# Kernel tuning notes

Hardware: AMD Instinct MI355X
Metric: run time of the kernel (lower is better)

The kernel has to match this reference:

```python
import jax, jax.numpy as jnp
import numpy as np

N_PTS0 = 32   # samples per line
N_PTS1 = 8    # after maxpool (scale factor 4)
DIM_LOI = 128
DIM_FC = 1024
FEAT_DIM = 8
HW = 128      # feature-map spatial size (hardcoded via clamp(max=127) in source)


def setup_inputs() -> dict:
    key = jax.random.key(0)
    ks = jax.random.split(key, 11)
    B, L = 8, 5000
    feature = jax.random.normal(ks[0], (B, 256, HW, HW), jnp.float32)
    # line endpoints in pixel coords [0, 128)
    p = jax.random.uniform(ks[1], (B, L, 2, 2), jnp.float32) * HW
    feat = jax.random.normal(ks[2], (B, L, FEAT_DIM), jnp.float32)
    W_fc1 = jax.random.normal(ks[3], (DIM_LOI, 256), jnp.float32) * 0.05
    b_fc1 = jnp.zeros((DIM_LOI,), jnp.float32)
    d_in = DIM_LOI * N_PTS1 + FEAT_DIM  # 1032
    W1 = jax.random.normal(ks[4], (d_in, DIM_FC), jnp.float32) * 0.03
    b1 = jnp.zeros((DIM_FC,), jnp.float32)
    W2 = jax.random.normal(ks[5], (DIM_FC, DIM_FC), jnp.float32) * 0.03
    b2 = jnp.zeros((DIM_FC,), jnp.float32)
    W3 = jax.random.normal(ks[6], (DIM_FC, 1), jnp.float32) * 0.03
    b3 = jnp.zeros((1,), jnp.float32)
    return dict(feature=feature, p=p, feat=feat, W_fc1=W_fc1, b_fc1=b_fc1,
                W1=W1, b1=b1, W2=W2, b2=b2, W3=W3, b3=b3)


def _loi_head(feature, p, feat, W_fc1, b_fc1, W1, b1, W2, b2, W3, b3):
    B, _, H, W = feature.shape
    L = p.shape[1]
    # fc1: 1x1 conv -> [B, DIM_LOI, H, W]
    x = jnp.einsum('bchw,dc->bdhw', feature, W_fc1) + b_fc1[None, :, None, None]

    # sample N_PTS0 points along each line: [B, L, 32, 2]
    lam = jnp.linspace(0.0, 1.0, N_PTS0, dtype=p.dtype)[:, None]
    pts = p[:, :, 0:1, :] * lam + p[:, :, 1:2, :] * (1.0 - lam) - 0.5
    px, py = pts[..., 0], pts[..., 1]
    px0 = jnp.clip(jnp.floor(px), 0.0, HW - 1)
    py0 = jnp.clip(jnp.floor(py), 0.0, HW - 1)
    px1 = jnp.clip(px0 + 1.0, 0.0, HW - 1)
    py1 = jnp.clip(py0 + 1.0, 0.0, HW - 1)
    px0i, py0i = px0.astype(jnp.int32), py0.astype(jnp.int32)
    px1i, py1i = px1.astype(jnp.int32), py1.astype(jnp.int32)

    # bilinear blend weights [B, L, 32] -> broadcast over channel dim
    w00 = ((px1 - px) * (py1 - py))[:, None]
    w10 = ((px - px0) * (py1 - py))[:, None]
    w01 = ((px1 - px) * (py - py0))[:, None]
    w11 = ((px - px0) * (py - py0))[:, None]

    gather = jax.vmap(lambda xb, ix, iy: xb[:, ix, iy])  # [C,L,32] per image
    xp = (gather(x, px0i, py0i) * w00 + gather(x, px1i, py0i) * w10 +
          gather(x, px0i, py1i) * w01 + gather(x, px1i, py1i) * w11)  # [B,C,L,32]
    xp = jnp.transpose(xp, (0, 2, 1, 3))  # [B, L, C, 32]

    # MaxPool1d(kernel=4, stride=4) over sampled points -> [B, L, C, 8]
    pooled = xp.reshape(B, L, DIM_LOI, N_PTS1, N_PTS0 // N_PTS1).max(-1)
    flat = pooled.reshape(B, L, DIM_LOI * N_PTS1)
    z = jnp.concatenate([flat, feat], axis=-1)  # [B, L, 1032]

    h = jax.nn.relu(z @ W1 + b1)
    h = jax.nn.relu(h @ W2 + b2)
    logits = (h @ W3 + b3)[..., 0]  # [B, L]
    return logits


def reference(feature, p, feat, W_fc1, b_fc1, W1, b1, W2, b2, W3, b3):
    return _loi_head(feature, p, feat, W_fc1, b_fc1, W1, b1, W2, b2, W3, b3)
```

## Files before the change

### kernel.cpp

```cpp
#include <hip/hip_runtime.h>

typedef _Float16 f16;
typedef __fp16 h16x2 __attribute__((ext_vector_type(2)));
typedef f16 f16x8 __attribute__((ext_vector_type(8)));
typedef float f32x4 __attribute__((ext_vector_type(4)));

#define HW    128
#define NPIX  16384
#define CDIM  256
#define DLOI  128
#define LROWS 40000
#define DFC   1024
#define KP1   1088

__global__ __launch_bounds__(256, 4) void conv1x1_kernel(
    const float* __restrict__ feature, const float* __restrict__ Wfc,
    const float* __restrict__ bfc, f16* __restrict__ x) {
  const int tid = threadIdx.x;
  const int l = tid & 63;
  const int w = tid >> 6;
  const int b = blockIdx.y;
  const int pix0 = blockIdx.x * 128;
  const int wr = (w >> 1) * 64;
  const int wc = (w & 1) * 64;
  const int lrow = l & 15;
  const int g4 = l >> 4;

  const float* fb = feature + (size_t)b * CDIM * NPIX;
  f32x4 acc[4][4] = {};

  for (int kf = 0; kf < 8; ++kf) {
    const int kb = kf * 32 + g4 * 8;
    f16x8 bf[4];
#pragma unroll
    for (int n = 0; n < 4; ++n) {
      const float* wp = &Wfc[(size_t)(wc + n * 16 + lrow) * CDIM + kb];
      float4 w0 = *(const float4*)wp;
      float4 w1 = *(const float4*)(wp + 4);
      union { f16x8 v; h16x2 h[4]; } u;
      u.h[0] = __builtin_amdgcn_cvt_pkrtz(w0.x, w0.y);
      u.h[1] = __builtin_amdgcn_cvt_pkrtz(w0.z, w0.w);
      u.h[2] = __builtin_amdgcn_cvt_pkrtz(w1.x, w1.y);
      u.h[3] = __builtin_amdgcn_cvt_pkrtz(w1.z, w1.w);
      bf[n] = u.v;
    }
#pragma unroll
    for (int m = 0; m < 4; ++m) {
      const int pix = pix0 + wr + m * 16 + lrow;
      const float* ap = fb + (size_t)kb * NPIX + pix;
      float av[8];
#pragma unroll
      for (int j = 0; j < 8; ++j) av[j] = ap[(size_t)j * NPIX];
      union { f16x8 v; h16x2 h[4]; } u;
      u.h[0] = __builtin_amdgcn_cvt_pkrtz(av[0], av[1]);
      u.h[1] = __builtin_amdgcn_cvt_pkrtz(av[2], av[3]);
      u.h[2] = __builtin_amdgcn_cvt_pkrtz(av[4], av[5]);
      u.h[3] = __builtin_amdgcn_cvt_pkrtz(av[6], av[7]);
#pragma unroll
      for (int n = 0; n < 4; ++n)
        acc[m][n] = __builtin_amdgcn_mfma_f32_16x16x32_f16(u.v, bf[n], acc[m][n], 0, 0, 0);
    }
  }

#pragma unroll
  for (int m = 0; m < 4; ++m) {
#pragma unroll
    for (int r = 0; r < 4; ++r) {
      const int pix = pix0 + wr + m * 16 + g4 * 4 + r;
      f16* xr = x + ((size_t)b * NPIX + pix) * DLOI;
#pragma unroll
      for (int n = 0; n < 4; ++n) {
        const int d = wc + n * 16 + lrow;
        xr[d] = (f16)(acc[m][n][r] + bfc[d]);
      }
    }
  }
}

__global__ __launch_bounds__(256) void sample_kernel(
    const f16* __restrict__ x, const float* __restrict__ p,
    const float* __restrict__ feat, f16* __restrict__ z) {
  const int tid = threadIdx.x;
  const int wv = tid >> 6;
  const int lane = tid & 63;
  const int sub = lane >> 4;
  const int cl = lane & 15;
  const int bid = blockIdx.x;
  const int b = bid & 7;
  const int row = b * 5000 + (bid >> 3) * 4 + wv;

  const float4 pe = *(const float4*)&p[(size_t)row * 4];
  const size_t bb = (size_t)b * NPIX;
  f16* zr = z + (size_t)row * KP1;

#pragma unroll
  for (int gh = 0; gh < 2; ++gh) {
    const int g = gh * 4 + sub;
    float acc[8];
#pragma unroll
    for (int ci = 0; ci < 8; ++ci) acc[ci] = -1e30f;
#pragma unroll
    for (int pt = 0; pt < 4; ++pt) {
      const int t = g * 4 + pt;
      const float lam = (float)t * (1.0f / 31.0f);
      const float px = pe.x * lam + pe.z * (1.f - lam) - 0.5f;
      const float py = pe.y * lam + pe.w * (1.f - lam) - 0.5f;
      const float px0 = fminf(fmaxf(floorf(px), 0.f), 127.f);
      const float py0 = fminf(fmaxf(floorf(py), 0.f), 127.f);
      const float px1 = fminf(px0 + 1.f, 127.f);
      const float py1 = fminf(py0 + 1.f, 127.f);
      const int ix0 = (int)px0, iy0 = (int)py0, ix1 = (int)px1, iy1 = (int)py1;
      const float w00 = (px1 - px) * (py1 - py);
      const float w10 = (px - px0) * (py1 - py);
      const float w01 = (px1 - px) * (py - py0);
      const float w11 = (px - px0) * (py - py0);

      const f16* r00 = x + (bb + ix0 * HW + iy0) * DLOI + cl * 8;
      const f16* r10 = x + (bb + ix1 * HW + iy0) * DLOI + cl * 8;
      const f16* r01 = x + (bb + ix0 * HW + iy1) * DLOI + cl * 8;
      const f16* r11 = x + (bb + ix1 * HW + iy1) * DLOI + cl * 8;
      f16x8 a  = *(const f16x8*)r00;
      f16x8 bq = *(const f16x8*)r10;
      f16x8 cq = *(const f16x8*)r01;
      f16x8 dq = *(const f16x8*)r11;
#pragma unroll
      for (int ci = 0; ci < 8; ++ci) {
        float m = w00 * (float)a[ci] + w10 * (float)bq[ci] +
                  w01 * (float)cq[ci] + w11 * (float)dq[ci];
        acc[ci] = fmaxf(acc[ci], m);
      }
    }
    f16x8 o;
#pragma unroll
    for (int ci = 0; ci < 8; ++ci) o[ci] = (f16)acc[ci];
    *(f16x8*)(zr + g * 128 + cl * 8) = o;
  }
  if (lane < 8) zr[1024 + lane] = (f16)feat[(size_t)row * 8 + lane];
  else if (lane < 36) *(unsigned int*)((char*)zr + 2064 + (lane - 8) * 4) = 0u;
}

__global__ __launch_bounds__(256) void wtrans_kernel(
    const float* __restrict__ W, f16* __restrict__ Wt, int K, int ldt, int permute) {
  __shared__ float t[32][33];
  const int tx = threadIdx.x & 31, ty = threadIdx.x >> 5;
#pragma unroll
  for (int i = 0; i < 4; ++i) {
    int kd = blockIdx.y * 32 + ty + i * 8;
    int ks = (permute && kd < 1024) ? ((kd & 127) * 8 + (kd >> 7)) : kd;
    int n = blockIdx.x * 32 + tx;
    t[ty + i * 8][tx] = (ks < K) ? W[(size_t)ks * DFC + n] : 0.f;
  }
  __syncthreads();
#pragma unroll
  for (int i = 0; i < 4; ++i) {
    int n = blockIdx.x * 32 + ty + i * 8;
    int k = blockIdx.y * 32 + tx;
    Wt[(size_t)n * ldt + k] = (f16)t[tx][ty + i * 8];
  }
}

__global__ __launch_bounds__(256) void gemm_f16(
    const f16* __restrict__ A, const f16* __restrict__ Bt,
    const float* __restrict__ bias, f16* __restrict__ C,
    int M, int ksteps, int lda) {
  __shared__ f16 As[128 * 64];
  __shared__ f16 Bs[128 * 64];
  const int tid = threadIdx.x;
  const int l = tid & 63;
  const int w = tid >> 6;

  const int nwg = gridDim.x;
  const int s = (blockIdx.x & 7) * (nwg >> 3) + (blockIdx.x >> 3);
  const int m0 = (s >> 3) * 128;
  const int n0 = (s & 7) * 128;

  const int wr = (w >> 1) * 64, wc = (w & 1) * 64;
  const int srow = w * 8 + (l >> 3);
  const int slot = l & 7;

  f32x4 acc[4][4] = {};

  for (int kt = 0; kt < ksteps; ++kt) {
    const int kb = kt * 64;
    __syncthreads();
#pragma unroll
    for (int c = 0; c < 4; ++c) {
      int row = c * 32 + srow;
      int arow = m0 + row; if (arow >= M) arow = M - 1;
      const f16* g = A + (size_t)arow * lda + kb + ((slot ^ (row & 7)) * 8);
      __builtin_amdgcn_global_load_lds(
          (const __attribute__((address_space(1))) void*)g,
          (__attribute__((address_space(3))) void*)(As + row * 64 + slot * 8),
          16, 0, 0);
    }
#pragma unroll
    for (int c = 0; c < 4; ++c) {
      int row = c * 32 + srow;
      const f16* g = Bt + (size_t)(n0 + row) * lda + kb + ((slot ^ (row & 7)) * 8);
      __builtin_amdgcn_global_load_lds(
          (const __attribute__((address_space(1))) void*)g,
          (__attribute__((address_space(3))) void*)(Bs + row * 64 + slot * 8),
          16, 0, 0);
    }
    __syncthreads();

    const int lrow = l & 15;
    const int g4 = l >> 4;
#pragma unroll
    for (int kh = 0; kh < 2; ++kh) {
      f16x8 af[4], bf[4];
#pragma unroll
      for (int m = 0; m < 4; ++m) {
        int row = wr + m * 16 + lrow;
        int sl = (g4 + 4 * kh) ^ (row & 7);
        af[m] = *(const f16x8*)(As + row * 64 + sl * 8);
      }
#pragma unroll
      for (int n = 0; n < 4; ++n) {
        int row = wc + n * 16 + lrow;
        int sl = (g4 + 4 * kh) ^ (row & 7);
        bf[n] = *(const f16x8*)(Bs + row * 64 + sl * 8);
      }
#pragma unroll
      for (int m = 0; m < 4; ++m)
#pragma unroll
        for (int n = 0; n < 4; ++n)
          acc[m][n] = __builtin_amdgcn_mfma_f32_16x16x32_f16(af[m], bf[n], acc[m][n], 0, 0, 0);
    }
  }

  const int ocol0 = n0 + wc + (l & 15);
  const int orow0 = m0 + wr + (l >> 4) * 4;
#pragma unroll
  for (int m = 0; m < 4; ++m) {
#pragma unroll
    for (int r = 0; r < 4; ++r) {
      int orow = orow0 + m * 16 + r;
      if (orow >= M) continue;
      f16* crow = C + (size_t)orow * DFC;
#pragma unroll
      for (int n = 0; n < 4; ++n) {
        int col = ocol0 + n * 16;
        float v = acc[m][n][r] + bias[col];
        crow[col] = (f16)fmaxf(v, 0.f);
      }
    }
  }
}

__global__ __launch_bounds__(256) void fc3_kernel(
    const f16* __restrict__ H, const float* __restrict__ W3,
    const float* __restrict__ b3, float* __restrict__ out, int M) {
  const int lane = threadIdx.x & 63;
  const int w = threadIdx.x >> 6;
  const int row = blockIdx.x * 4 + w;
  if (row >= M) return;
  const f16* hr = H + (size_t)row * DFC;
  float s = 0.f;
#pragma unroll
  for (int k = 0; k < 2; ++k) {
    int j = (lane + k * 64) * 8;
    f16x8 hv = *(const f16x8*)&hr[j];
    float4 w0 = *(const float4*)&W3[j];
    float4 w1 = *(const float4*)&W3[j + 4];
    s += (float)hv[0] * w0.x + (float)hv[1] * w0.y +
         (float)hv[2] * w0.z + (float)hv[3] * w0.w +
         (float)hv[4] * w1.x + (float)hv[5] * w1.y +
         (float)hv[6] * w1.z + (float)hv[7] * w1.w;
  }
  for (int off = 32; off; off >>= 1) s += __shfl_xor(s, off);
  if (lane == 0) out[row] = s + b3[0];
}

extern "C" void kernel_launch(void* const* d_in, const int* in_sizes, int n_in,
                              void* d_out, int out_size, void* d_ws, size_t ws_size,
                              hipStream_t stream) {
  const float* feature = (const float*)d_in[0];
  const float* p       = (const float*)d_in[1];
  const float* feat    = (const float*)d_in[2];
  const float* W_fc1   = (const float*)d_in[3];
  const float* b_fc1   = (const float*)d_in[4];
  const float* W1      = (const float*)d_in[5];
  const float* b1      = (const float*)d_in[6];
  const float* W2      = (const float*)d_in[7];
  const float* b2      = (const float*)d_in[8];
  const float* W3      = (const float*)d_in[9];
  const float* b3      = (const float*)d_in[10];
  float* out = (float*)d_out;

  char* ws = (char*)d_ws;
  f16* x   = (f16*)(ws + 0);
  f16* z   = (f16*)(ws + 33554432ULL);
  f16* h1  = (f16*)(ws + 120594432ULL);
  f16* W1t = (f16*)(ws + 202514432ULL);
  f16* W2t = (f16*)(ws + 204742656ULL);
  f16* h2  = z;

  hipLaunchKernelGGL(wtrans_kernel, dim3(32, 34), dim3(256), 0, stream,
                     W1, W1t, 1032, KP1, 1);
  hipLaunchKernelGGL(wtrans_kernel, dim3(32, 32), dim3(256), 0, stream,
                     W2, W2t, 1024, 1024, 0);
  hipLaunchKernelGGL(conv1x1_kernel, dim3(128, 8), dim3(256), 0, stream,
                     feature, W_fc1, b_fc1, x);
  hipLaunchKernelGGL(sample_kernel, dim3(10000), dim3(256), 0, stream,
                     x, p, feat, z);
  hipLaunchKernelGGL(gemm_f16, dim3(2504), dim3(256), 0, stream,
                     z, W1t, b1, h1, LROWS, KP1 / 64, KP1);
  hipLaunchKernelGGL(gemm_f16, dim3(2504), dim3(256), 0, stream,
                     h1, W2t, b2, h2, LROWS, DFC / 64, DFC);
  hipLaunchKernelGGL(fc3_kernel, dim3(10000), dim3(256), 0, stream,
                     h2, W3, b3, out, LROWS);
}
```

Baseline: 380.3 us.

## Replace 128x128 GEMM with double-buffered 256x256 tile, 8-wave pingpong kernel

Swaps the f16 MFMA GEMM used for both MLP layers from a 128x128 tile with 4 waves and a single LDS buffer to a 256x256 tile with 8 waves and double-buffered LDS. Loads for the next K step are split into four quarter stages, each interleaved with one compute phase and fenced by barriers and priority changes, so global-to-LDS copies overlap MFMA work. The larger tile raises arithmetic intensity and cuts the grid from 2504 to 628 workgroups. In exchange it uses more registers (128 accumulator floats per lane) and 128KB of LDS, relies on hand-placed waitcnt and barrier scheduling, and wastes more work on the partial last M tile.

```diff
diff --git a/kernel.cpp b/kernel.cpp
--- a/kernel.cpp
+++ b/kernel.cpp
@@ -159,89 +159,129 @@
   }
 }
 
-__global__ __launch_bounds__(256) void gemm_f16(
+template <int MH, int NH>
+__device__ __forceinline__ void phase_compute(
+    const f16* __restrict__ AsB, const f16* __restrict__ BsB,
+    f32x4 (&acc)[8][4], int wm, int wn, int lrow, int g4) {
+  f16x8 af[4][2], bf[2][2];
+#pragma unroll
+  for (int mf = 0; mf < 4; ++mf)
+#pragma unroll
+    for (int kk = 0; kk < 2; ++kk) {
+      int row = wm * 128 + (MH * 4 + mf) * 16 + lrow;
+      int sl = (kk * 4 + g4) ^ (row & 7);
+      af[mf][kk] = *(const f16x8*)(AsB + row * 64 + sl * 8);
+    }
+#pragma unroll
+  for (int nf = 0; nf < 2; ++nf)
+#pragma unroll
+    for (int kk = 0; kk < 2; ++kk) {
+      int row = wn * 64 + (NH * 2 + nf) * 16 + lrow;
+      int sl = (kk * 4 + g4) ^ (row & 7);
+      bf[nf][kk] = *(const f16x8*)(BsB + row * 64 + sl * 8);
+    }
+  __builtin_amdgcn_s_barrier();
+  __builtin_amdgcn_sched_barrier(0);
+  __builtin_amdgcn_s_setprio(1);
+#pragma unroll
+  for (int kk = 0; kk < 2; ++kk)
+#pragma unroll
+    for (int mf = 0; mf < 4; ++mf)
+#pragma unroll
+      for (int nf = 0; nf < 2; ++nf)
+        acc[MH * 4 + mf][NH * 2 + nf] = __builtin_amdgcn_mfma_f32_16x16x32_f16(
+            af[mf][kk], bf[nf][kk], acc[MH * 4 + mf][NH * 2 + nf], 0, 0, 0);
+  __builtin_amdgcn_s_setprio(0);
+  __builtin_amdgcn_s_barrier();
+  __builtin_amdgcn_sched_barrier(0);
+}
+
+__global__ __launch_bounds__(512, 2) void gemm256(
     const f16* __restrict__ A, const f16* __restrict__ Bt,
     const float* __restrict__ bias, f16* __restrict__ C,
     int M, int ksteps, int lda) {
-  __shared__ f16 As[128 * 64];
-  __shared__ f16 Bs[128 * 64];
+  __shared__ f16 As[2][256 * 64];
+  __shared__ f16 Bs[2][256 * 64];
   const int tid = threadIdx.x;
   const int l = tid & 63;
   const int w = tid >> 6;
+  const int wm = w >> 2, wn = w & 3;
+  const int lrow = l & 15, g4 = l >> 4;
 
   const int nwg = gridDim.x;
-  const int s = (blockIdx.x & 7) * (nwg >> 3) + (blockIdx.x >> 3);
-  const int m0 = (s >> 3) * 128;
-  const int n0 = (s & 7) * 128;
-
-  const int wr = (w >> 1) * 64, wc = (w & 1) * 64;
-  const int srow = w * 8 + (l >> 3);
-  const int slot = l & 7;
-
-  f32x4 acc[4][4] = {};
-
-  for (int kt = 0; kt < ksteps; ++kt) {
-    const int kb = kt * 64;
-    __syncthreads();
-#pragma unroll
-    for (int c = 0; c < 4; ++c) {
-      int row = c * 32 + srow;
-      int arow = m0 + row; if (arow >= M) arow = M - 1;
-      const f16* g = A + (size_t)arow * lda + kb + ((slot ^ (row & 7)) * 8);
+  const int q = nwg >> 3, r = nwg & 7;
+  const int xcd = blockIdx.x & 7, idx = blockIdx.x >> 3;
+  const int wgid = (xcd < r ? xcd * (q + 1) : r * (q + 1) + (xcd - r) * q) + idx;
+  const int m0 = (wgid >> 2) * 256;
+  const int n0 = (wgid & 3) * 256;
+
+  const int srow0 = tid >> 3;
+  const int sslot = tid & 7;
+
+  f32x4 acc[8][4] = {};
+
+  auto stage_A = [&](int buf, int half, int kb) {
+#pragma unroll
+    for (int rr = 0; rr < 2; ++rr) {
+      int row = rr * 64 + srow0;
+      int grow = m0 + half * 128 + row;
+      if (grow >= M) grow = M - 1;
+      const f16* g = A + (size_t)grow * lda + kb + ((sslot ^ (row & 7)) * 8);
       __builtin_amdgcn_global_load_lds(
           (const __attribute__((address_space(1))) void*)g,
-          (__attribute__((address_space(3))) void*)(As + row * 64 + slot * 8),
+          (__attribute__((address_space(3))) void*)(&As[buf][(half * 128 + row) * 64 + sslot * 8]),
           16, 0, 0);
     }
-#pragma unroll
-    for (int c = 0; c < 4; ++c) {
-      int row = c * 32 + srow;
-      const f16* g = Bt + (size_t)(n0 + row) * lda + kb + ((slot ^ (row & 7)) * 8);
+  };
+  auto stage_B = [&](int buf, int half, int kb) {
+#pragma unroll
+    for (int rr = 0; rr < 2; ++rr) {
+      int row = rr * 64 + srow0;
+      int grow = n0 + half * 128 + row;
+      const f16* g = Bt + (size_t)grow * lda + kb + ((sslot ^ (row & 7)) * 8);
       __builtin_amdgcn_global_load_lds(
           (const __attribute__((address_space(1))) void*)g,
-          (__attribute__((address_space(3))) void*)(Bs + row * 64 + slot * 8),
+          (__attribute__((address_space(3))) void*)(&Bs[buf][(half * 128 + row) * 64 + sslot * 8]),
           16, 0, 0);
     }
-    __syncthreads();
-
-    const int lrow = l & 15;
-    const int g4 = l >> 4;
-#pragma unroll
-    for (int kh = 0; kh < 2; ++kh) {
-      f16x8 af[4], bf[4];
-#pragma unroll
-      for (int m = 0; m < 4; ++m) {
-        int row = wr + m * 16 + lrow;
-        int sl = (g4 + 4 * kh) ^ (row & 7);
-        af[m] = *(const f16x8*)(As + row * 64 + sl * 8);
-      }
-#pragma unroll
-      for (int n = 0; n < 4; ++n) {
-        int row = wc + n * 16 + lrow;
-        int sl = (g4 + 4 * kh) ^ (row & 7);
-        bf[n] = *(const f16x8*)(Bs + row * 64 + sl * 8);
-      }
-#pragma unroll
-      for (int m = 0; m < 4; ++m)
-#pragma unroll
-        for (int n = 0; n < 4; ++n)
-          acc[m][n] = __builtin_amdgcn_mfma_f32_16x16x32_f16(af[m], bf[n], acc[m][n], 0, 0, 0);
-    }
-  }
-
-  const int ocol0 = n0 + wc + (l & 15);
-  const int orow0 = m0 + wr + (l >> 4) * 4;
-#pragma unroll
-  for (int m = 0; m < 4; ++m) {
-#pragma unroll
-    for (int r = 0; r < 4; ++r) {
-      int orow = orow0 + m * 16 + r;
+  };
+
+  stage_A(0, 0, 0); stage_A(0, 1, 0); stage_B(0, 0, 0); stage_B(0, 1, 0);
+
+  for (int kt = 0; kt < ksteps; ++kt) {
+    const int buf = kt & 1;
+    const int nbuf = buf ^ 1;
+    const int kb2 = (kt + 1 < ksteps ? kt + 1 : kt) * 64;
+    const f16* AsB = &As[buf][0];
+    const f16* BsB = &Bs[buf][0];
+
+    stage_A(nbuf, 0, kb2);
+    asm volatile("s_waitcnt vmcnt(2)" ::: "memory");
+    __builtin_amdgcn_s_barrier();
+    __builtin_amdgcn_sched_barrier(0);
+    phase_compute<0, 0>(AsB, BsB, acc, wm, wn, lrow, g4);
+
+    stage_A(nbuf, 1, kb2);
+    phase_compute<0, 1>(AsB, BsB, acc, wm, wn, lrow, g4);
+
+    stage_B(nbuf, 0, kb2);
+    phase_compute<1, 0>(AsB, BsB, acc, wm, wn, lrow, g4);
+
+    stage_B(nbuf, 1, kb2);
+    phase_compute<1, 1>(AsB, BsB, acc, wm, wn, lrow, g4);
+  }
+
+#pragma unroll
+  for (int mf = 0; mf < 8; ++mf) {
+#pragma unroll
+    for (int rr = 0; rr < 4; ++rr) {
+      int orow = m0 + wm * 128 + mf * 16 + g4 * 4 + rr;
       if (orow >= M) continue;
       f16* crow = C + (size_t)orow * DFC;
 #pragma unroll
-      for (int n = 0; n < 4; ++n) {
-        int col = ocol0 + n * 16;
-        float v = acc[m][n][r] + bias[col];
+      for (int nf = 0; nf < 4; ++nf) {
+        int col = n0 + wn * 64 + nf * 16 + lrow;
+        float v = acc[mf][nf][rr] + bias[col];
         crow[col] = (f16)fmaxf(v, 0.f);
       }
     }
@@ -304,9 +344,9 @@
                      feature, W_fc1, b_fc1, x);
   hipLaunchKernelGGL(sample_kernel, dim3(10000), dim3(256), 0, stream,
                      x, p, feat, z);
-  hipLaunchKernelGGL(gemm_f16, dim3(2504), dim3(256), 0, stream,
+  hipLaunchKernelGGL(gemm256, dim3(628), dim3(512), 0, stream,
                      z, W1t, b1, h1, LROWS, KP1 / 64, KP1);
-  hipLaunchKernelGGL(gemm_f16, dim3(2504), dim3(256), 0, stream,
+  hipLaunchKernelGGL(gemm256, dim3(628), dim3(512), 0, stream,
                      h1, W2t, b2, h2, LROWS, DFC / 64, DFC);
   hipLaunchKernelGGL(fc3_kernel, dim3(10000), dim3(256), 0, stream,
                      h2, W3, b3, out, LROWS);
```

Result: slower. 522.0 us (+37.3%).

## Fuse fc3 dot product into second GEMM epilogue with atomic accumulation

Applied to the files above, without the earlier changes.

The second FC GEMM now applies bias and ReLU, multiplies by W3 in registers, reduces across lanes with shuffles, and atomically adds partial row sums into the output. This removes the write and re-read of the 40000x1024 f16 h2 activation and the separate fc3 launch. A small fill kernel first initialises the output with b3. The cost is 8 column-tile atomics per row and a float summation order that is no longer deterministic.

```diff
diff --git a/kernel.cpp b/kernel.cpp
--- a/kernel.cpp
+++ b/kernel.cpp
@@ -248,28 +248,108 @@
   }
 }
 
-__global__ __launch_bounds__(256) void fc3_kernel(
-    const f16* __restrict__ H, const float* __restrict__ W3,
-    const float* __restrict__ b3, float* __restrict__ out, int M) {
-  const int lane = threadIdx.x & 63;
-  const int w = threadIdx.x >> 6;
-  const int row = blockIdx.x * 4 + w;
-  if (row >= M) return;
-  const f16* hr = H + (size_t)row * DFC;
-  float s = 0.f;
-#pragma unroll
-  for (int k = 0; k < 2; ++k) {
-    int j = (lane + k * 64) * 8;
-    f16x8 hv = *(const f16x8*)&hr[j];
-    float4 w0 = *(const float4*)&W3[j];
-    float4 w1 = *(const float4*)&W3[j + 4];
-    s += (float)hv[0] * w0.x + (float)hv[1] * w0.y +
-         (float)hv[2] * w0.z + (float)hv[3] * w0.w +
-         (float)hv[4] * w1.x + (float)hv[5] * w1.y +
-         (float)hv[6] * w1.z + (float)hv[7] * w1.w;
-  }
-  for (int off = 32; off; off >>= 1) s += __shfl_xor(s, off);
-  if (lane == 0) out[row] = s + b3[0];
+__global__ __launch_bounds__(256) void gemm2_fc3(
+    const f16* __restrict__ A, const f16* __restrict__ Bt,
+    const float* __restrict__ bias, const float* __restrict__ W3,
+    float* __restrict__ out, int M, int ksteps, int lda) {
+  __shared__ f16 As[128 * 64];
+  __shared__ f16 Bs[128 * 64];
+  const int tid = threadIdx.x;
+  const int l = tid & 63;
+  const int w = tid >> 6;
+
+  const int nwg = gridDim.x;
+  const int s = (blockIdx.x & 7) * (nwg >> 3) + (blockIdx.x >> 3);
+  const int m0 = (s >> 3) * 128;
+  const int n0 = (s & 7) * 128;
+
+  const int wr = (w >> 1) * 64, wc = (w & 1) * 64;
+  const int srow = w * 8 + (l >> 3);
+  const int slot = l & 7;
+
+  f32x4 acc[4][4] = {};
+
+  for (int kt = 0; kt < ksteps; ++kt) {
+    const int kb = kt * 64;
+    __syncthreads();
+#pragma unroll
+    for (int c = 0; c < 4; ++c) {
+      int row = c * 32 + srow;
+      int arow = m0 + row; if (arow >= M) arow = M - 1;
+      const f16* g = A + (size_t)arow * lda + kb + ((slot ^ (row & 7)) * 8);
+      __builtin_amdgcn_global_load_lds(
+          (const __attribute__((address_space(1))) void*)g,
+          (__attribute__((address_space(3))) void*)(As + row * 64 + slot * 8),
+          16, 0, 0);
+    }
+#pragma unroll
+    for (int c = 0; c < 4; ++c) {
+      int row = c * 32 + srow;
+      const f16* g = Bt + (size_t)(n0 + row) * lda + kb + ((slot ^ (row & 7)) * 8);
+      __builtin_amdgcn_global_load_lds(
+          (const __attribute__((address_space(1))) void*)g,
+          (__attribute__((address_space(3))) void*)(Bs + row * 64 + slot * 8),
+          16, 0, 0);
+    }
+    __syncthreads();
+
+    const int lrow = l & 15;
+    const int g4 = l >> 4;
+#pragma unroll
+    for (int kh = 0; kh < 2; ++kh) {
+      f16x8 af[4], bf[4];
+#pragma unroll
+      for (int m = 0; m < 4; ++m) {
+        int row = wr + m * 16 + lrow;
+        int sl = (g4 + 4 * kh) ^ (row & 7);
+        af[m] = *(const f16x8*)(As + row * 64 + sl * 8);
+      }
+#pragma unroll
+      for (int n = 0; n < 4; ++n) {
+        int row = wc + n * 16 + lrow;
+        int sl = (g4 + 4 * kh) ^ (row & 7);
+        bf[n] = *(const f16x8*)(Bs + row * 64 + sl * 8);
+      }
+#pragma unroll
+      for (int m = 0; m < 4; ++m)
+#pragma unroll
+        for (int n = 0; n < 4; ++n)
+          acc[m][n] = __builtin_amdgcn_mfma_f32_16x16x32_f16(af[m], bf[n], acc[m][n], 0, 0, 0);
+    }
+  }
+
+  const int ocol0 = n0 + wc + (l & 15);
+  const int orow0 = m0 + wr + (l >> 4) * 4;
+  float b4[4], w3v[4];
+#pragma unroll
+  for (int n = 0; n < 4; ++n) {
+    b4[n] = bias[ocol0 + n * 16];
+    w3v[n] = W3[ocol0 + n * 16];
+  }
+#pragma unroll
+  for (int m = 0; m < 4; ++m) {
+#pragma unroll
+    for (int r = 0; r < 4; ++r) {
+      float sacc = 0.f;
+#pragma unroll
+      for (int n = 0; n < 4; ++n) {
+        float v = fmaxf(acc[m][n][r] + b4[n], 0.f);
+        sacc += v * w3v[n];
+      }
+      sacc += __shfl_xor(sacc, 1);
+      sacc += __shfl_xor(sacc, 2);
+      sacc += __shfl_xor(sacc, 4);
+      sacc += __shfl_xor(sacc, 8);
+      int orow = orow0 + m * 16 + r;
+      if ((l & 15) == 0 && orow < M) atomicAdd(&out[orow], sacc);
+    }
+  }
+}
+
+__global__ __launch_bounds__(256) void fill_out(
+    float* __restrict__ out, const float* __restrict__ b3, int n) {
+  int i = blockIdx.x * 256 + threadIdx.x;
+  if (i < n) out[i] = b3[0];
 }
 
 extern "C" void kernel_launch(void* const* d_in, const int* in_sizes, int n_in,
@@ -294,7 +374,6 @@
   f16* h1  = (f16*)(ws + 120594432ULL);
   f16* W1t = (f16*)(ws + 202514432ULL);
   f16* W2t = (f16*)(ws + 204742656ULL);
-  f16* h2  = z;
 
   hipLaunchKernelGGL(wtrans_kernel, dim3(32, 34), dim3(256), 0, stream,
                      W1, W1t, 1032, KP1, 1);
@@ -306,8 +385,8 @@
                      x, p, feat, z);
   hipLaunchKernelGGL(gemm_f16, dim3(2504), dim3(256), 0, stream,
                      z, W1t, b1, h1, LROWS, KP1 / 64, KP1);
-  hipLaunchKernelGGL(gemm_f16, dim3(2504), dim3(256), 0, stream,
-                     h1, W2t, b2, h2, LROWS, DFC / 64, DFC);
-  hipLaunchKernelGGL(fc3_kernel, dim3(10000), dim3(256), 0, stream,
-                     h2, W3, b3, out, LROWS);
-}
+  hipLaunchKernelGGL(fill_out, dim3(157), dim3(256), 0, stream,
+                     out, b3, LROWS);
+  hipLaunchKernelGGL(gemm2_fc3, dim3(2504), dim3(256), 0, stream,
+                     h1, W2t, b2, W3, out, LROWS, DFC / 64, DFC);
+}
```

New measurement: 364.4 us. 4.2% less time.

## Double-buffer GEMM with 32x32 MFMA and fuse fc3 into second GEMM epilogue

Applied to the files above, without the earlier changes.

Rewrites the f16 GEMM main loop to double-buffer the LDS tiles, issuing the next k-step's global-to-LDS loads before computing the current one, and switches from 16x16x32 to 32x32x16 MFMA with fewer LDS fragment reads. The second GEMM no longer writes h2; its epilogue applies bias and ReLU, multiplies by W3, reduces across lanes and atomically adds into the output, which a new fill kernel initialises with b3. This removes the h2 round trip and the separate fc3 launch, at the cost of doubled LDS use, atomics, and reduction order that is no longer deterministic.

```diff
diff --git a/kernel.cpp b/kernel.cpp
--- a/kernel.cpp
+++ b/kernel.cpp
@@ -4,6 +4,7 @@
 typedef __fp16 h16x2 __attribute__((ext_vector_type(2)));
 typedef f16 f16x8 __attribute__((ext_vector_type(8)));
 typedef float f32x4 __attribute__((ext_vector_type(4)));
+typedef float f32x16 __attribute__((ext_vector_type(16)));
 
 #define HW    128
 #define NPIX  16384
@@ -159,117 +160,125 @@
   }
 }
 
-__global__ __launch_bounds__(256) void gemm_f16(
+#define GEMM_MAIN_LOOP(A_, Bt_, M_, ksteps_, lda_)                              \
+  __shared__ f16 As[2][128 * 64];                                               \
+  __shared__ f16 Bs[2][128 * 64];                                               \
+  const int tid = threadIdx.x;                                                  \
+  const int l = tid & 63;                                                       \
+  const int w = tid >> 6;                                                       \
+  const int nwg = gridDim.x;                                                    \
+  const int s = (blockIdx.x & 7) * (nwg >> 3) + (blockIdx.x >> 3);              \
+  const int m0 = (s >> 3) * 128;                                                \
+  const int n0 = (s & 7) * 128;                                                 \
+  const int wr = (w >> 1) * 64, wc = (w & 1) * 64;                              \
+  const int srow = w * 8 + (l >> 3);                                            \
+  const int slot = l & 7;                                                       \
+  const int l31 = l & 31, l5 = l >> 5;                                          \
+  f32x16 acc[2][2] = {};                                                        \
+  auto stage = [&](int bi, int kb) {                                            \
+    _Pragma("unroll")                                                           \
+    for (int c = 0; c < 4; ++c) {                                               \
+      int row = c * 32 + srow;                                                  \
+      int arow = m0 + row; if (arow >= M_) arow = M_ - 1;                       \
+      const f16* g = A_ + (size_t)arow * lda_ + kb + ((slot ^ (row & 7)) * 8);  \
+      __builtin_amdgcn_global_load_lds(                                         \
+          (const __attribute__((address_space(1))) void*)g,                     \
+          (__attribute__((address_space(3))) void*)(&As[bi][row * 64 + slot * 8]), \
+          16, 0, 0);                                                            \
+    }                                                                           \
+    _Pragma("unroll")                                                           \
+    for (int c = 0; c < 4; ++c) {                                               \
+      int row = c * 32 + srow;                                                  \
+      const f16* g = Bt_ + (size_t)(n0 + row) * lda_ + kb + ((slot ^ (row & 7)) * 8); \
+      __builtin_amdgcn_global_load_lds(                                         \
+          (const __attribute__((address_space(1))) void*)g,                     \
+          (__attribute__((address_space(3))) void*)(&Bs[bi][row * 64 + slot * 8]), \
+          16, 0, 0);                                                            \
+    }                                                                           \
+  };                                                                            \
+  stage(0, 0);                                                                  \
+  for (int kt = 0; kt < ksteps_; ++kt) {                                        \
+    const int kb2 = (kt + 1 < ksteps_ ? kt + 1 : kt) * 64;                      \
+    stage((kt + 1) & 1, kb2);                                                   \
+    asm volatile("s_waitcnt vmcnt(8)" ::: "memory");                            \
+    __builtin_amdgcn_s_barrier();                                               \
+    __builtin_amdgcn_sched_barrier(0);                                          \
+    const f16* AsB = &As[kt & 1][0];                                            \
+    const f16* BsB = &Bs[kt & 1][0];                                            \
+    _Pragma("unroll")                                                           \
+    for (int kq = 0; kq < 4; ++kq) {                                            \
+      f16x8 af0, af1, bf0, bf1;                                                 \
+      {                                                                         \
+        int rowa0 = wr + l31;                                                   \
+        int rowa1 = wr + 32 + l31;                                              \
+        int rowb0 = wc + l31;                                                   \
+        int rowb1 = wc + 32 + l31;                                              \
+        int sl = kq * 2 + l5;                                                   \
+        af0 = *(const f16x8*)(AsB + rowa0 * 64 + (sl ^ (rowa0 & 7)) * 8);       \
+        af1 = *(const f16x8*)(AsB + rowa1 * 64 + (sl ^ (rowa1 & 7)) * 8);       \
+        bf0 = *(const f16x8*)(BsB + rowb0 * 64 + (sl ^ (rowb0 & 7)) * 8);       \
+        bf1 = *(const f16x8*)(BsB + rowb1 * 64 + (sl ^ (rowb1 & 7)) * 8);       \
+      }                                                                         \
+      acc[0][0] = __builtin_amdgcn_mfma_f32_32x32x16_f16(af0, bf0, acc[0][0], 0, 0, 0); \
+      acc[0][1] = __builtin_amdgcn_mfma_f32_32x32x16_f16(af0, bf1, acc[0][1], 0, 0, 0); \
+      acc[1][0] = __builtin_amdgcn_mfma_f32_32x32x16_f16(af1, bf0, acc[1][0], 0, 0, 0); \
+      acc[1][1] = __builtin_amdgcn_mfma_f32_32x32x16_f16(af1, bf1, acc[1][1], 0, 0, 0); \
+    }                                                                           \
+    __builtin_amdgcn_sched_barrier(0);                                          \
+    __builtin_amdgcn_s_barrier();                                               \
+  }
+
+__global__ __launch_bounds__(256, 2) void gemm_f16(
     const f16* __restrict__ A, const f16* __restrict__ Bt,
     const float* __restrict__ bias, f16* __restrict__ C,
     int M, int ksteps, int lda) {
-  __shared__ f16 As[128 * 64];
-  __shared__ f16 Bs[128 * 64];
-  const int tid = threadIdx.x;
-  const int l = tid & 63;
-  const int w = tid >> 6;
-
-  const int nwg = gridDim.x;
-  const int s = (blockIdx.x & 7) * (nwg >> 3) + (blockIdx.x >> 3);
-  const int m0 = (s >> 3) * 128;
-  const int n0 = (s & 7) * 128;
-
-  const int wr = (w >> 1) * 64, wc = (w & 1) * 64;
-  const int srow = w * 8 + (l >> 3);
-  const int slot = l & 7;
-
-  f32x4 acc[4][4] = {};
-
-  for (int kt = 0; kt < ksteps; ++kt) {
-    const int kb = kt * 64;
-    __syncthreads();
-#pragma unroll
-    for (int c = 0; c < 4; ++c) {
-      int row = c * 32 + srow;
-      int arow = m0 + row; if (arow >= M) arow = M - 1;
-      const f16* g = A + (size_t)arow * lda + kb + ((slot ^ (row & 7)) * 8);
-      __builtin_amdgcn_global_load_lds(
-          (const __attribute__((address_space(1))) void*)g,
-          (__attribute__((address_space(3))) void*)(As + row * 64 + slot * 8),
-          16, 0, 0);
-    }
-#pragma unroll
-    for (int c = 0; c < 4; ++c) {
-      int row = c * 32 + srow;
-      const f16* g = Bt + (size_t)(n0 + row) * lda + kb + ((slot ^ (row & 7)) * 8);
-      __builtin_amdgcn_global_load_lds(
-          (const __attribute__((address_space(1))) void*)g,
-          (__attribute__((address_space(3))) void*)(Bs + row * 64 + slot * 8),
-          16, 0, 0);
-    }
-    __syncthreads();
-
-    const int lrow = l & 15;
-    const int g4 = l >> 4;
-#pragma unroll
-    for (int kh = 0; kh < 2; ++kh) {
-      f16x8 af[4], bf[4];
-#pragma unroll
-      for (int m = 0; m < 4; ++m) {
-        int row = wr + m * 16 + lrow;
-        int sl = (g4 + 4 * kh) ^ (row & 7);
-        af[m] = *(const f16x8*)(As + row * 64 + sl * 8);
-      }
-#pragma unroll
-      for (int n = 0; n < 4; ++n) {
-        int row = wc + n * 16 + lrow;
-        int sl = (g4 + 4 * kh) ^ (row & 7);
-        bf[n] = *(const f16x8*)(Bs + row * 64 + sl * 8);
-      }
-#pragma unroll
-      for (int m = 0; m < 4; ++m)
-#pragma unroll
-        for (int n = 0; n < 4; ++n)
-          acc[m][n] = __builtin_amdgcn_mfma_f32_16x16x32_f16(af[m], bf[n], acc[m][n], 0, 0, 0);
-    }
-  }
-
-  const int ocol0 = n0 + wc + (l & 15);
-  const int orow0 = m0 + wr + (l >> 4) * 4;
-#pragma unroll
-  for (int m = 0; m < 4; ++m) {
-#pragma unroll
-    for (int r = 0; r < 4; ++r) {
-      int orow = orow0 + m * 16 + r;
-      if (orow >= M) continue;
-      f16* crow = C + (size_t)orow * DFC;
-#pragma unroll
-      for (int n = 0; n < 4; ++n) {
-        int col = ocol0 + n * 16;
-        float v = acc[m][n][r] + bias[col];
-        crow[col] = (f16)fmaxf(v, 0.f);
-      }
-    }
-  }
-}
-
-__global__ __launch_bounds__(256) void fc3_kernel(
-    const f16* __restrict__ H, const float* __restrict__ W3,
-    const float* __restrict__ b3, float* __restrict__ out, int M) {
-  const int lane = threadIdx.x & 63;
-  const int w = threadIdx.x >> 6;
-  const int row = blockIdx.x * 4 + w;
-  if (row >= M) return;
-  const f16* hr = H + (size_t)row * DFC;
-  float s = 0.f;
-#pragma unroll
-  for (int k = 0; k < 2; ++k) {
-    int j = (lane + k * 64) * 8;
-    f16x8 hv = *(const f16x8*)&hr[j];
-    float4 w0 = *(const float4*)&W3[j];
-    float4 w1 = *(const float4*)&W3[j + 4];
-    s += (float)hv[0] * w0.x + (float)hv[1] * w0.y +
-         (float)hv[2] * w0.z + (float)hv[3] * w0.w +
-         (float)hv[4] * w1.x + (float)hv[5] * w1.y +
-         (float)hv[6] * w1.z + (float)hv[7] * w1.w;
-  }
-  for (int off = 32; off; off >>= 1) s += __shfl_xor(s, off);
-  if (lane == 0) out[row] = s + b3[0];
+  GEMM_MAIN_LOOP(A, Bt, M, ksteps, lda)
+
+  const int colb = n0 + wc + l31;
+  float b0 = bias[colb], b1 = bias[colb + 32];
+#pragma unroll
+  for (int mf = 0; mf < 2; ++mf) {
+#pragma unroll
+    for (int reg = 0; reg < 16; ++reg) {
+      int row = m0 + wr + mf * 32 + (reg & 3) + 8 * (reg >> 2) + 4 * l5;
+      if (row >= M) continue;
+      f16* crow = C + (size_t)row * DFC;
+      crow[colb]      = (f16)fmaxf(acc[mf][0][reg] + b0, 0.f);
+      crow[colb + 32] = (f16)fmaxf(acc[mf][1][reg] + b1, 0.f);
+    }
+  }
+}
+
+__global__ __launch_bounds__(256, 2) void gemm2_fc3(
+    const f16* __restrict__ A, const f16* __restrict__ Bt,
+    const float* __restrict__ bias, const float* __restrict__ W3,
+    float* __restrict__ out, int M, int ksteps, int lda) {
+  GEMM_MAIN_LOOP(A, Bt, M, ksteps, lda)
+
+  const int colb = n0 + wc + l31;
+  float b0 = bias[colb], b1 = bias[colb + 32];
+  float w30 = W3[colb], w31 = W3[colb + 32];
+#pragma unroll
+  for (int mf = 0; mf < 2; ++mf) {
+#pragma unroll
+    for (int reg = 0; reg < 16; ++reg) {
+      float sacc = fmaxf(acc[mf][0][reg] + b0, 0.f) * w30 +
+                   fmaxf(acc[mf][1][reg] + b1, 0.f) * w31;
+      sacc += __shfl_xor(sacc, 1);
+      sacc += __shfl_xor(sacc, 2);
+      sacc += __shfl_xor(sacc, 4);
+      sacc += __shfl_xor(sacc, 8);
+      sacc += __shfl_xor(sacc, 16);
+      int row = m0 + wr + mf * 32 + (reg & 3) + 8 * (reg >> 2) + 4 * l5;
+      if (l31 == 0 && row < M) atomicAdd(&out[row], sacc);
+    }
+  }
+}
+
+__global__ __launch_bounds__(256) void fill_out(
+    float* __restrict__ out, const float* __restrict__ b3, int n) {
+  int i = blockIdx.x * 256 + threadIdx.x;
+  if (i < n) out[i] = b3[0];
 }
 
 extern "C" void kernel_launch(void* const* d_in, const int* in_sizes, int n_in,
@@ -294,7 +303,6 @@
   f16* h1  = (f16*)(ws + 120594432ULL);
   f16* W1t = (f16*)(ws + 202514432ULL);
   f16* W2t = (f16*)(ws + 204742656ULL);
-  f16* h2  = z;
 
   hipLaunchKernelGGL(wtrans_kernel, dim3(32, 34), dim3(256), 0, stream,
                      W1, W1t, 1032, KP1, 1);
@@ -306,8 +314,8 @@
                      x, p, feat, z);
   hipLaunchKernelGGL(gemm_f16, dim3(2504), dim3(256), 0, stream,
                      z, W1t, b1, h1, LROWS, KP1 / 64, KP1);
-  hipLaunchKernelGGL(gemm_f16, dim3(2504), dim3(256), 0, stream,
-                     h1, W2t, b2, h2, LROWS, DFC / 64, DFC);
-  hipLaunchKernelGGL(fc3_kernel, dim3(10000), dim3(256), 0, stream,
-                     h2, W3, b3, out, LROWS);
-}
+  hipLaunchKernelGGL(fill_out, dim3(157), dim3(256), 0, stream,
+                     out, b3, LROWS);
+  hipLaunchKernelGGL(gemm2_fc3, dim3(2504), dim3(256), 0, stream,
+                     h1, W2t, b2, W3, out, LROWS, DFC / 64, DFC);
+}
```

Result: slower. 422.2 us (+11.0%).
